# Performance work log

Measured on AMD Instinct MI355X. Metric: run time of the kernel, lower is better.

## Reference

```python
import jax, jax.numpy as jnp
import numpy as np

NUM_EXPERTS = 8
TOP_K = 2
D_IN = 1024
D_OUT = 1024
N_TOKENS = 8192


def setup_inputs() -> dict:
    key = jax.random.key(0)
    ks = jax.random.split(key, 7)
    s_in = 1.0 / np.sqrt(D_IN)
    s_out = 1.0 / np.sqrt(D_OUT)
    return {
        "x": jax.random.normal(ks[0], (N_TOKENS, D_IN), dtype=jnp.float32),
        # stacked expert params: fc1 [E, D_in, D_out], fc2 [E, D_out, D_out]
        "W1": jax.random.uniform(ks[1], (NUM_EXPERTS, D_IN, D_OUT), jnp.float32, -s_in, s_in),
        "b1": jax.random.uniform(ks[2], (NUM_EXPERTS, D_OUT), jnp.float32, -s_in, s_in),
        "W2": jax.random.uniform(ks[3], (NUM_EXPERTS, D_OUT, D_OUT), jnp.float32, -s_out, s_out),
        "b2": jax.random.uniform(ks[4], (NUM_EXPERTS, D_OUT), jnp.float32, -s_out, s_out),
        "Wg": jax.random.uniform(ks[5], (D_IN, NUM_EXPERTS), jnp.float32, -s_in, s_in),
        "bg": jax.random.uniform(ks[6], (NUM_EXPERTS,), jnp.float32, -s_in, s_in),
    }


def reference(x, W1, b1, W2, b2, Wg, bg):
    n = x.shape[0]
    # gating
    gate_logits = x @ Wg + bg                      # [N, E]
    gate_weights = jax.nn.softmax(gate_logits, axis=1)
    if TOP_K < NUM_EXPERTS:
        topk_vals, topk_idx = jax.lax.top_k(gate_weights, TOP_K)  # [N, K]
        rows = jnp.arange(n)[:, None]
        gate_weights = jnp.zeros_like(gate_weights).at[rows, topk_idx].set(topk_vals)
    # dense all-expert MLP fan-out (faithful to the original wasteful compute)
    h = jax.nn.relu(jnp.einsum('nd,edh->enh', x, W1) + b1[:, None, :])  # [E, N, H]
    y = jnp.einsum('enh,eho->eno', h, W2) + b2[:, None, :]               # [E, N, O]
    # weighted combine over experts
    out = jnp.einsum('ne,eno->no', gate_weights, y)                      # [N, O]
    return out
```

## Files before the change

kernel.cpp:

```cpp
#include <hip/hip_runtime.h>

#define NUM_E 8
#define N_TOK 8192
#define DIM 1024

typedef __attribute__((ext_vector_type(8))) short short8;
typedef __attribute__((ext_vector_type(4))) float f32x4;

__device__ __forceinline__ unsigned short f2bf(float f) {
  unsigned int u = __float_as_uint(f);
  u = (u + 0x7fffu + ((u >> 16) & 1u)) >> 16;
  return (unsigned short)u;
}

__device__ __forceinline__ void async16(const unsigned short* g, unsigned short* l) {
  __builtin_amdgcn_global_load_lds((const __attribute__((address_space(1))) void*)g,
                                   (__attribute__((address_space(3))) void*)l,
                                   16, 0, 0);
}

__global__ __launch_bounds__(256) void convert_w_kernel(const float* __restrict__ W1,
                                                        const float* __restrict__ W2,
                                                        unsigned short* __restrict__ W1T,
                                                        unsigned short* __restrict__ W2T) {
  int tid = blockIdx.x * 256 + threadIdx.x;
  int n   = tid & 1023;
  int kc  = (tid >> 10) & 127;
  int mat = tid >> 17;
  const float* src;
  unsigned short* dst;
  if (mat < 8) { src = W1 + (size_t)mat * (DIM * DIM); dst = W1T + (size_t)mat * (DIM * DIM); }
  else         { src = W2 + (size_t)(mat - 8) * (DIM * DIM); dst = W2T + (size_t)(mat - 8) * (DIM * DIM); }
  const int k0 = kc * 8;
  union { unsigned short u[8]; uint4 v; } o;
#pragma unroll
  for (int j = 0; j < 8; ++j)
    o.u[j] = f2bf(src[(size_t)(k0 + j) * DIM + n]);
  *(uint4*)(dst + (size_t)n * DIM + k0) = o.v;
}

__global__ __launch_bounds__(256) void gate1_kernel(const float* __restrict__ x,
                                                    const float* __restrict__ Wg,
                                                    const float* __restrict__ bg,
                                                    int* __restrict__ tok_top,
                                                    float2* __restrict__ tok_wts,
                                                    unsigned short* __restrict__ xb) {
  const int wave = threadIdx.x >> 6;
  const int lane = threadIdx.x & 63;
  const int n = blockIdx.x * 4 + wave;
  const float4* xr = (const float4*)(x + (size_t)n * DIM);
  unsigned short* xbr = xb + (size_t)n * DIM;
  float acc[NUM_E];
#pragma unroll
  for (int e = 0; e < NUM_E; ++e) acc[e] = 0.f;
#pragma unroll
  for (int it = 0; it < 4; ++it) {
    float4 xv = xr[it * 64 + lane];
    const float4* wr = (const float4*)Wg + (size_t)(it * 256 + lane * 4) * 2;
    float xs[4] = {xv.x, xv.y, xv.z, xv.w};
    union { unsigned short u[4]; uint2 v; } oo;
    oo.u[0] = f2bf(xv.x); oo.u[1] = f2bf(xv.y);
    oo.u[2] = f2bf(xv.z); oo.u[3] = f2bf(xv.w);
    *(uint2*)(xbr + it * 256 + lane * 4) = oo.v;
#pragma unroll
    for (int dd = 0; dd < 4; ++dd) {
      float4 wa = wr[dd * 2 + 0];
      float4 wb = wr[dd * 2 + 1];
      acc[0] += xs[dd] * wa.x; acc[1] += xs[dd] * wa.y;
      acc[2] += xs[dd] * wa.z; acc[3] += xs[dd] * wa.w;
      acc[4] += xs[dd] * wb.x; acc[5] += xs[dd] * wb.y;
      acc[6] += xs[dd] * wb.z; acc[7] += xs[dd] * wb.w;
    }
  }
#pragma unroll
  for (int e = 0; e < NUM_E; ++e)
#pragma unroll
    for (int off = 32; off > 0; off >>= 1)
      acc[e] += __shfl_down(acc[e], off);
  if (lane == 0) {
    float p[NUM_E];
    float mx = -1e30f;
#pragma unroll
    for (int e = 0; e < NUM_E; ++e) { p[e] = acc[e] + bg[e]; mx = fmaxf(mx, p[e]); }
    float s = 0.f;
#pragma unroll
    for (int e = 0; e < NUM_E; ++e) { p[e] = expf(p[e] - mx); s += p[e]; }
    float inv = 1.f / s;
    int i0 = 0;
#pragma unroll
    for (int e = 1; e < NUM_E; ++e) if (p[e] > p[i0]) i0 = e;
    int i1 = (i0 == 0) ? 1 : 0;
#pragma unroll
    for (int e = 0; e < NUM_E; ++e) if (e != i0 && p[e] > p[i1]) i1 = e;
    tok_top[n] = i0 | (i1 << 8);
    tok_wts[n] = make_float2(p[i0] * inv, p[i1] * inv);
  }
}

__global__ __launch_bounds__(1024) void gate2_kernel(const int* __restrict__ tok_top,
                                                     const float2* __restrict__ tok_wts,
                                                     int* __restrict__ counts,
                                                     int* __restrict__ tok_idx,
                                                     float* __restrict__ tok_w) {
  const int e = blockIdx.x;
  const int t = threadIdx.x;
  const int lane = t & 63;
  const int wave = t >> 6;
  __shared__ int wsum[16];
  __shared__ int blocktot;
  int match[8];
  float w[8];
  int cnt = 0;
#pragma unroll
  for (int j = 0; j < 8; ++j) {
    int n = t * 8 + j;
    int top = tok_top[n];
    float2 ww = tok_wts[n];
    bool m0 = (top & 0xff) == e;
    bool m1 = ((top >> 8) & 0xff) == e;
    match[j] = (m0 || m1) ? 1 : 0;
    w[j] = m0 ? ww.x : ww.y;
    cnt += match[j];
  }
  int inc = cnt;
#pragma unroll
  for (int off = 1; off < 64; off <<= 1) {
    int v = __shfl_up(inc, off);
    if (lane >= off) inc += v;
  }
  if (lane == 63) wsum[wave] = inc;
  __syncthreads();
  if (t < 16) {
    int v = wsum[t];
    int s = v;
#pragma unroll
    for (int off = 1; off < 16; off <<= 1) {
      int u = __shfl_up(s, off);
      if (lane >= off) s += u;
    }
    wsum[t] = s - v;
    if (t == 15) blocktot = s;
  }
  __syncthreads();
  int slot = wsum[wave] + inc - cnt;
#pragma unroll
  for (int j = 0; j < 8; ++j) {
    if (match[j]) {
      tok_idx[e * N_TOK + slot] = t * 8 + j;
      tok_w[e * N_TOK + slot] = w[j];
      slot++;
    }
  }
  if (t == 0) counts[e] = blocktot;
}


template <bool FC1>
__global__ __launch_bounds__(256, 3) void moe_gemm_kernel(
    const unsigned short* __restrict__ A_src,
    const unsigned short* __restrict__ wT,
    const float* __restrict__ bias,
    const int* __restrict__ counts,
    const int* __restrict__ tok_idx,
    const float* __restrict__ tok_w,
    unsigned short* __restrict__ h_out,
    float* __restrict__ out)
{
  const int e = blockIdx.x;
  const int count = counts[e];
  const int m0 = blockIdx.z * 128;
  if (m0 >= count) return;
  const int n0 = blockIdx.y * 128;

  int base = 0;
#pragma unroll
  for (int i = 0; i < NUM_E; ++i) base += (i < e) ? ((counts[i] + 127) & ~127) : 0;

  const int tid  = threadIdx.x;
  const int wave = tid >> 6;
  const int lane = tid & 63;
  const int l15  = lane & 15;
  const int quad = lane >> 4;
  const int wm   = wave & 1;
  const int wn   = wave >> 1;

  __shared__ unsigned short sA[3][128 * 32];
  __shared__ unsigned short sB[3][128 * 32];
  __shared__ int   s_tok[128];
  __shared__ float s_w[128];

  if (!FC1) {
    if (tid < 128) {
      int slot = m0 + tid;
      int cs = slot < count ? slot : count - 1;
      s_tok[tid] = tok_idx[e * N_TOK + cs];
      s_w[tid]   = slot < count ? tok_w[e * N_TOK + slot] : 0.f;
    }
    __syncthreads();
  }

  const int r0 = 32 * wave + l15;
  const int r1 = r0 + 16;
  size_t aOff0, aOff1;
  if (FC1) {
    int s0 = m0 + r0; s0 = s0 < count ? s0 : count - 1;
    int s1 = m0 + r1; s1 = s1 < count ? s1 : count - 1;
    aOff0 = (size_t)tok_idx[e * N_TOK + s0] * DIM;
    aOff1 = (size_t)tok_idx[e * N_TOK + s1] * DIM;
  } else {
    aOff0 = (size_t)(base + m0 + r0) * DIM;
    aOff1 = (size_t)(base + m0 + r1) * DIM;
  }
  const unsigned short* wte = wT + (size_t)e * DIM * DIM;
  const size_t bOff0 = (size_t)(n0 + r0) * DIM;
  const size_t bOff1 = (size_t)(n0 + r1) * DIM;
  const int kl = quad * 8;
  const int c0 = (2 * wave + 0) * 512;
  const int c1 = (2 * wave + 1) * 512;

  const f32x4 vzero = {0.f, 0.f, 0.f, 0.f};
  f32x4 acc[4][4];
#pragma unroll
  for (int i = 0; i < 4; ++i)
#pragma unroll
    for (int j = 0; j < 4; ++j) acc[i][j] = vzero;

  auto stage = [&](int kt, int b) {
    const int koff = kt * 32 + kl;
    async16(A_src + aOff0 + koff, &sA[b][c0]);
    async16(A_src + aOff1 + koff, &sA[b][c1]);
    async16(wte + bOff0 + koff, &sB[b][c0]);
    async16(wte + bOff1 + koff, &sB[b][c1]);
  };

  stage(0, 0);
  stage(1, 1);
#pragma unroll
  for (int kt = 0; kt < 32; ++kt) {
    const int cur = kt % 3;
    if (kt + 1 < 32) {
      asm volatile("s_waitcnt vmcnt(4)\n\ts_barrier" ::: "memory");
    } else {
      asm volatile("s_waitcnt vmcnt(0)\n\ts_barrier" ::: "memory");
    }
    if (kt + 2 < 32) stage(kt + 2, (kt + 2) % 3);
    short8 af[4], bfr[4];
#pragma unroll
    for (int i = 0; i < 4; ++i)
      af[i] = *(const short8*)&sA[cur][(wm * 4 + i) * 512 + lane * 8];
#pragma unroll
    for (int j = 0; j < 4; ++j)
      bfr[j] = *(const short8*)&sB[cur][(wn * 4 + j) * 512 + lane * 8];
#pragma unroll
    for (int i = 0; i < 4; ++i)
#pragma unroll
      for (int j = 0; j < 4; ++j)
        acc[i][j] = __builtin_amdgcn_mfma_f32_16x16x32_bf16(af[i], bfr[j], acc[i][j], 0, 0, 0);
  }

  float bv[4];
#pragma unroll
  for (int j = 0; j < 4; ++j)
    bv[j] = bias[e * DIM + n0 + (wn * 4 + j) * 16 + l15];

  if (FC1) {
#pragma unroll
    for (int i = 0; i < 4; ++i) {
      const int rbase = (wm * 4 + i) * 16 + quad * 4;
#pragma unroll
      for (int r = 0; r < 4; ++r) {
        const int slot = m0 + rbase + r;
        if (slot < count) {
          unsigned short* hp = h_out + (size_t)(base + slot) * DIM + n0;
#pragma unroll
          for (int j = 0; j < 4; ++j) {
            float v = acc[i][j][r] + bv[j];
            v = v > 0.f ? v : 0.f;
            hp[(wn * 4 + j) * 16 + l15] = f2bf(v);
          }
        }
      }
    }
  } else {
#pragma unroll
    for (int i = 0; i < 4; ++i) {
      const int rbase = (wm * 4 + i) * 16 + quad * 4;
#pragma unroll
      for (int r = 0; r < 4; ++r) {
        const int slot = m0 + rbase + r;
        if (slot < count) {
          const int rl = rbase + r;
          const int tok = s_tok[rl];
          const float w = s_w[rl];
          float* op = out + (size_t)tok * DIM + n0;
#pragma unroll
          for (int j = 0; j < 4; ++j) {
            float v = acc[i][j][r] + bv[j];
            atomicAdd(&op[(wn * 4 + j) * 16 + l15], w * v);
          }
        }
      }
    }
  }
}


extern "C" void kernel_launch(void* const* d_in, const int* in_sizes, int n_in,
                              void* d_out, int out_size, void* d_ws, size_t ws_size,
                              hipStream_t stream) {
  const float* x  = (const float*)d_in[0];
  const float* W1 = (const float*)d_in[1];
  const float* b1 = (const float*)d_in[2];
  const float* W2 = (const float*)d_in[3];
  const float* b2 = (const float*)d_in[4];
  const float* Wg = (const float*)d_in[5];
  const float* bg = (const float*)d_in[6];
  float* out = (float*)d_out;

  char* ws = (char*)d_ws;
  int*            counts  = (int*)(ws);
  int*            tok_idx = (int*)(ws + 1024);
  float*          tok_w   = (float*)(ws + 263168);
  unsigned short* xb      = (unsigned short*)(ws + 525312);
  unsigned short* w1t     = (unsigned short*)(ws + 525312 + 16777216ull);
  unsigned short* w2t     = (unsigned short*)(ws + 525312 + 2ull * 16777216ull);
  unsigned short* hb      = (unsigned short*)(ws + 525312 + 3ull * 16777216ull);
  size_t gate_off = 525312 + 3ull * 16777216ull + 35651584ull;
  int*            tok_top = (int*)(ws + gate_off);
  float2*         tok_wts = (float2*)(ws + gate_off + 32768);

  hipMemsetAsync(d_out, 0, (size_t)N_TOK * DIM * sizeof(float), stream);

  convert_w_kernel<<<2 * NUM_E * DIM * (DIM / 8) / 256, 256, 0, stream>>>(W1, W2, w1t, w2t);
  gate1_kernel<<<N_TOK / 4, 256, 0, stream>>>(x, Wg, bg, tok_top, tok_wts, xb);
  gate2_kernel<<<NUM_E, 1024, 0, stream>>>(tok_top, tok_wts, counts, tok_idx, tok_w);
  moe_gemm_kernel<true><<<dim3(NUM_E, 8, 64), 256, 0, stream>>>(
      xb, w1t, b1, counts, tok_idx, tok_w, hb, nullptr);
  moe_gemm_kernel<false><<<dim3(NUM_E, 8, 64), 256, 0, stream>>>(
      hb, w2t, b2, counts, tok_idx, tok_w, nullptr, out);
}
```

Before: 398.8 us.

## Tile weight transpose through LDS; switch MoE GEMM to single-wave register-direct tiles

New measurement: 504.7 us. +26.6%, slower.

```diff
diff --git a/kernel.cpp b/kernel.cpp
--- a/kernel.cpp
+++ b/kernel.cpp
@@ -13,30 +13,37 @@
   return (unsigned short)u;
 }
 
-__device__ __forceinline__ void async16(const unsigned short* g, unsigned short* l) {
-  __builtin_amdgcn_global_load_lds((const __attribute__((address_space(1))) void*)g,
-                                   (__attribute__((address_space(3))) void*)l,
-                                   16, 0, 0);
-}
-
 __global__ __launch_bounds__(256) void convert_w_kernel(const float* __restrict__ W1,
                                                         const float* __restrict__ W2,
                                                         unsigned short* __restrict__ W1T,
                                                         unsigned short* __restrict__ W2T) {
-  int tid = blockIdx.x * 256 + threadIdx.x;
-  int n   = tid & 1023;
-  int kc  = (tid >> 10) & 127;
-  int mat = tid >> 17;
+  const int bx  = blockIdx.x;
+  const int mat = bx >> 8;
+  const int tk  = (bx >> 4) & 15;
+  const int tn  = bx & 15;
   const float* src;
   unsigned short* dst;
   if (mat < 8) { src = W1 + (size_t)mat * (DIM * DIM); dst = W1T + (size_t)mat * (DIM * DIM); }
   else         { src = W2 + (size_t)(mat - 8) * (DIM * DIM); dst = W2T + (size_t)(mat - 8) * (DIM * DIM); }
-  const int k0 = kc * 8;
-  union { unsigned short u[8]; uint4 v; } o;
-#pragma unroll
-  for (int j = 0; j < 8; ++j)
-    o.u[j] = f2bf(src[(size_t)(k0 + j) * DIM + n]);
-  *(uint4*)(dst + (size_t)n * DIM + k0) = o.v;
+  const int k0 = tk * 64, n0 = tn * 64;
+  const int t = threadIdx.x;
+  __shared__ float s[64][65];
+  const int nr = t & 63, wr = t >> 6;
+#pragma unroll
+  for (int i = 0; i < 16; ++i) {
+    int k = i * 4 + wr;
+    s[nr][k] = src[(size_t)(k0 + k) * DIM + n0 + nr];
+  }
+  __syncthreads();
+  const int kq = (t & 15) * 4, nw = t >> 4;
+#pragma unroll
+  for (int i = 0; i < 4; ++i) {
+    int n = i * 16 + nw;
+    ushort4 o;
+    o.x = f2bf(s[n][kq + 0]); o.y = f2bf(s[n][kq + 1]);
+    o.z = f2bf(s[n][kq + 2]); o.w = f2bf(s[n][kq + 3]);
+    *(ushort4*)(dst + (size_t)(n0 + n) * DIM + k0 + kq) = o;
+  }
 }
 
 __global__ __launch_bounds__(256) void gate1_kernel(const float* __restrict__ x,
@@ -156,7 +163,7 @@
 
 
 template <bool FC1>
-__global__ __launch_bounds__(256, 3) void moe_gemm_kernel(
+__global__ __launch_bounds__(64, 2) void moe_gemm_kernel(
     const unsigned short* __restrict__ A_src,
     const unsigned short* __restrict__ wT,
     const float* __restrict__ bias,
@@ -168,55 +175,31 @@
 {
   const int e = blockIdx.x;
   const int count = counts[e];
-  const int m0 = blockIdx.z * 128;
+  const int m0 = blockIdx.z * 64;
   if (m0 >= count) return;
-  const int n0 = blockIdx.y * 128;
+  const int n0 = blockIdx.y * 64;
 
   int base = 0;
 #pragma unroll
-  for (int i = 0; i < NUM_E; ++i) base += (i < e) ? ((counts[i] + 127) & ~127) : 0;
-
-  const int tid  = threadIdx.x;
-  const int wave = tid >> 6;
-  const int lane = tid & 63;
+  for (int i = 0; i < NUM_E; ++i) base += (i < e) ? ((counts[i] + 63) & ~63) : 0;
+
+  const int lane = threadIdx.x;
   const int l15  = lane & 15;
   const int quad = lane >> 4;
-  const int wm   = wave & 1;
-  const int wn   = wave >> 1;
-
-  __shared__ unsigned short sA[3][128 * 32];
-  __shared__ unsigned short sB[3][128 * 32];
-  __shared__ int   s_tok[128];
-  __shared__ float s_w[128];
-
-  if (!FC1) {
-    if (tid < 128) {
-      int slot = m0 + tid;
-      int cs = slot < count ? slot : count - 1;
-      s_tok[tid] = tok_idx[e * N_TOK + cs];
-      s_w[tid]   = slot < count ? tok_w[e * N_TOK + slot] : 0.f;
-    }
-    __syncthreads();
-  }
-
-  const int r0 = 32 * wave + l15;
-  const int r1 = r0 + 16;
-  size_t aOff0, aOff1;
-  if (FC1) {
-    int s0 = m0 + r0; s0 = s0 < count ? s0 : count - 1;
-    int s1 = m0 + r1; s1 = s1 < count ? s1 : count - 1;
-    aOff0 = (size_t)tok_idx[e * N_TOK + s0] * DIM;
-    aOff1 = (size_t)tok_idx[e * N_TOK + s1] * DIM;
-  } else {
-    aOff0 = (size_t)(base + m0 + r0) * DIM;
-    aOff1 = (size_t)(base + m0 + r1) * DIM;
-  }
+
+  const unsigned short* ap[4];
+  const unsigned short* bp[4];
   const unsigned short* wte = wT + (size_t)e * DIM * DIM;
-  const size_t bOff0 = (size_t)(n0 + r0) * DIM;
-  const size_t bOff1 = (size_t)(n0 + r1) * DIM;
-  const int kl = quad * 8;
-  const int c0 = (2 * wave + 0) * 512;
-  const int c1 = (2 * wave + 1) * 512;
+#pragma unroll
+  for (int i = 0; i < 4; ++i) {
+    int s = m0 + i * 16 + l15;
+    s = s < count ? s : count - 1;
+    int row = FC1 ? tok_idx[e * N_TOK + s] : (base + s);
+    ap[i] = A_src + (size_t)row * DIM + quad * 8;
+  }
+#pragma unroll
+  for (int j = 0; j < 4; ++j)
+    bp[j] = wte + (size_t)(n0 + j * 16 + l15) * DIM + quad * 8;
 
   const f32x4 vzero = {0.f, 0.f, 0.f, 0.f};
   f32x4 acc[4][4];
@@ -225,48 +208,45 @@
 #pragma unroll
     for (int j = 0; j < 4; ++j) acc[i][j] = vzero;
 
-  auto stage = [&](int kt, int b) {
-    const int koff = kt * 32 + kl;
-    async16(A_src + aOff0 + koff, &sA[b][c0]);
-    async16(A_src + aOff1 + koff, &sA[b][c1]);
-    async16(wte + bOff0 + koff, &sB[b][c0]);
-    async16(wte + bOff1 + koff, &sB[b][c1]);
-  };
-
-  stage(0, 0);
-  stage(1, 1);
-#pragma unroll
-  for (int kt = 0; kt < 32; ++kt) {
-    const int cur = kt % 3;
-    if (kt + 1 < 32) {
-      asm volatile("s_waitcnt vmcnt(4)\n\ts_barrier" ::: "memory");
-    } else {
-      asm volatile("s_waitcnt vmcnt(0)\n\ts_barrier" ::: "memory");
-    }
-    if (kt + 2 < 32) stage(kt + 2, (kt + 2) % 3);
-    short8 af[4], bfr[4];
+  short8 a0[4], b0[4], a1[4], b1[4];
+#pragma unroll
+  for (int i = 0; i < 4; ++i) a0[i] = *(const short8*)(ap[i]);
+#pragma unroll
+  for (int j = 0; j < 4; ++j) b0[j] = *(const short8*)(bp[j]);
+
+#pragma unroll
+  for (int kt = 0; kt < 32; kt += 2) {
+#pragma unroll
+    for (int i = 0; i < 4; ++i) a1[i] = *(const short8*)(ap[i] + (kt + 1) * 32);
+#pragma unroll
+    for (int j = 0; j < 4; ++j) b1[j] = *(const short8*)(bp[j] + (kt + 1) * 32);
 #pragma unroll
     for (int i = 0; i < 4; ++i)
-      af[i] = *(const short8*)&sA[cur][(wm * 4 + i) * 512 + lane * 8];
-#pragma unroll
-    for (int j = 0; j < 4; ++j)
-      bfr[j] = *(const short8*)&sB[cur][(wn * 4 + j) * 512 + lane * 8];
+#pragma unroll
+      for (int j = 0; j < 4; ++j)
+        acc[i][j] = __builtin_amdgcn_mfma_f32_16x16x32_bf16(a0[i], b0[j], acc[i][j], 0, 0, 0);
+    if (kt + 2 < 32) {
+#pragma unroll
+      for (int i = 0; i < 4; ++i) a0[i] = *(const short8*)(ap[i] + (kt + 2) * 32);
+#pragma unroll
+      for (int j = 0; j < 4; ++j) b0[j] = *(const short8*)(bp[j] + (kt + 2) * 32);
+    }
 #pragma unroll
     for (int i = 0; i < 4; ++i)
 #pragma unroll
       for (int j = 0; j < 4; ++j)
-        acc[i][j] = __builtin_amdgcn_mfma_f32_16x16x32_bf16(af[i], bfr[j], acc[i][j], 0, 0, 0);
+        acc[i][j] = __builtin_amdgcn_mfma_f32_16x16x32_bf16(a1[i], b1[j], acc[i][j], 0, 0, 0);
   }
 
   float bv[4];
 #pragma unroll
   for (int j = 0; j < 4; ++j)
-    bv[j] = bias[e * DIM + n0 + (wn * 4 + j) * 16 + l15];
+    bv[j] = bias[e * DIM + n0 + j * 16 + l15];
 
   if (FC1) {
 #pragma unroll
     for (int i = 0; i < 4; ++i) {
-      const int rbase = (wm * 4 + i) * 16 + quad * 4;
+      const int rbase = i * 16 + quad * 4;
 #pragma unroll
       for (int r = 0; r < 4; ++r) {
         const int slot = m0 + rbase + r;
@@ -276,7 +256,7 @@
           for (int j = 0; j < 4; ++j) {
             float v = acc[i][j][r] + bv[j];
             v = v > 0.f ? v : 0.f;
-            hp[(wn * 4 + j) * 16 + l15] = f2bf(v);
+            hp[j * 16 + l15] = f2bf(v);
           }
         }
       }
@@ -284,19 +264,18 @@
   } else {
 #pragma unroll
     for (int i = 0; i < 4; ++i) {
-      const int rbase = (wm * 4 + i) * 16 + quad * 4;
+      const int rbase = i * 16 + quad * 4;
 #pragma unroll
       for (int r = 0; r < 4; ++r) {
         const int slot = m0 + rbase + r;
         if (slot < count) {
-          const int rl = rbase + r;
-          const int tok = s_tok[rl];
-          const float w = s_w[rl];
+          const int tok = tok_idx[e * N_TOK + slot];
+          const float w = tok_w[e * N_TOK + slot];
           float* op = out + (size_t)tok * DIM + n0;
 #pragma unroll
           for (int j = 0; j < 4; ++j) {
             float v = acc[i][j][r] + bv[j];
-            atomicAdd(&op[(wn * 4 + j) * 16 + l15], w * v);
+            atomicAdd(&op[j * 16 + l15], w * v);
           }
         }
       }
@@ -331,11 +310,11 @@
 
   hipMemsetAsync(d_out, 0, (size_t)N_TOK * DIM * sizeof(float), stream);
 
-  convert_w_kernel<<<2 * NUM_E * DIM * (DIM / 8) / 256, 256, 0, stream>>>(W1, W2, w1t, w2t);
+  convert_w_kernel<<<16 * 16 * 16, 256, 0, stream>>>(W1, W2, w1t, w2t);
   gate1_kernel<<<N_TOK / 4, 256, 0, stream>>>(x, Wg, bg, tok_top, tok_wts, xb);
   gate2_kernel<<<NUM_E, 1024, 0, stream>>>(tok_top, tok_wts, counts, tok_idx, tok_w);
-  moe_gemm_kernel<true><<<dim3(NUM_E, 8, 64), 256, 0, stream>>>(
+  moe_gemm_kernel<true><<<dim3(NUM_E, 16, 128), 64, 0, stream>>>(
       xb, w1t, b1, counts, tok_idx, tok_w, hb, nullptr);
-  moe_gemm_kernel<false><<<dim3(NUM_E, 8, 64), 256, 0, stream>>>(
+  moe_gemm_kernel<false><<<dim3(NUM_E, 16, 128), 64, 0, stream>>>(
       hb, w2t, b2, counts, tok_idx, tok_w, nullptr, out);
 }
```
